# Performance work log

Hardware: AMD Instinct MI355X
Metric: run time of the kernel (lower is better)

## Reference

```python
import jax, jax.numpy as jnp
import numpy as np


def _conv3x3(x, w, b):
    # NCHW conv, stride 1, padding 1 == SAME for 3x3
    y = jax.lax.conv_general_dilated(
        x, w, window_strides=(1, 1), padding='SAME',
        dimension_numbers=('NCHW', 'OIHW', 'NCHW'))
    return y + b[None, :, None, None]


def setup_inputs() -> dict:
    key = jax.random.key(0)
    k_x, k_w1, k_b1, k_w2, k_b2 = jax.random.split(key, 5)
    B, T, C, H, W = 4, 16, 128, 112, 112  # C = 2 * in_channels
    x = jax.random.normal(k_x, (B, T, C, H, W), dtype=jnp.float32)
    # PredictorLG_conv(embed_dim=2*in_channels): Conv2d(128,2,3) -> GELU -> Conv2d(2,2,3) -> GELU -> Softmax(dim=1)
    w1 = jax.random.normal(k_w1, (2, C, 3, 3), dtype=jnp.float32) * 0.05
    b1 = jax.random.normal(k_b1, (2,), dtype=jnp.float32) * 0.05
    w2 = jax.random.normal(k_w2, (2, 2, 3, 3), dtype=jnp.float32) * 0.05
    b2 = jax.random.normal(k_b2, (2,), dtype=jnp.float32) * 0.05
    return {"x": x, "w1": w1, "b1": b1, "w2": w2, "b2": b2}


def reference(x, w1, b1, w2, b2):
    # spatch branch of PatchNet_ms_conv.forward
    B, T, C, H, W = x.shape
    xf = x.reshape(B * T, C, H, W)  # (b t c h w) -> ((b t) c h w)
    s = jax.nn.gelu(_conv3x3(xf, w1, b1), approximate=False)
    s = jax.nn.gelu(_conv3x3(s, w2, b2), approximate=False)
    s = jax.nn.softmax(s, axis=1)  # nn.Softmax() on 4D -> dim=1
    x1, x2 = jnp.split(xf, 2, axis=1)  # chunk(2, dim=-3)
    xa = s[:, 0:1] * x1 + s[:, 1:2] * x2  # ((b t), c//2, h, w)
    # '(b t) c h w -> b c t h w'
    xa = xa.reshape(B, T, C // 2, H, W).transpose(0, 2, 1, 3, 4)
    return xa
```

## Files before the change

### kernel.cpp

```cpp
#include <hip/hip_runtime.h>
#include <math.h>
#include <stdint.h>

#define HW    112
#define HW2   (112 * 112)
#define NIMG  64
#define CIN   128
#define NKG   4
#define ICG   (CIN / NKG)
#define TILEF (18 * HW)
#define TILEP 2032

__device__ __forceinline__ float gelu_exact(float v) {
    return 0.5f * v * (1.0f + erff(v * 0.70710678118654752f));
}

__global__ __launch_bounds__(256) void k1_partial(
    const float* __restrict__ x, const float* __restrict__ w1,
    float* __restrict__ part) {
    __shared__ __align__(16) float tile[2][TILEP];

    const int tid = threadIdx.x;
    const int bx  = blockIdx.x;
    const int n   = blockIdx.y;
    const int kg  = blockIdx.z;
    const int h0  = bx * 16;
    const int icb = kg * ICG;

    const int tx   = tid & 15;
    const int ty   = tid >> 4;
    const int col0 = tx * 7;

    if (bx == 0 && tid < HW) { tile[0][tid] = 0.f; tile[1][tid] = 0.f; }
    if (bx == 6 && tid < HW) { tile[0][17 * HW + tid] = 0.f; tile[1][17 * HW + tid] = 0.f; }

    const int    ldsoff = (bx == 0) ? HW : 0;
    const int    count4 = (bx == 0 || bx == 6) ? 476 : 504;
    const size_t srcoff = (bx == 0) ? 0 : (size_t)(h0 - 1) * HW;
    const float* xn = x + ((size_t)n * CIN + icb) * HW2 + srcoff;

    const float lmask = (col0 > 0) ? 1.f : 0.f;
    const float rmask = (col0 + 7 < HW) ? 1.f : 0.f;
    const int   loff  = (col0 > 0) ? -1 : 0;
    const int   roff  = (col0 + 7 < HW) ? 7 : 0;

    float acc0[7] = {0.f, 0.f, 0.f, 0.f, 0.f, 0.f, 0.f};
    float acc1[7] = {0.f, 0.f, 0.f, 0.f, 0.f, 0.f, 0.f};

    {
        float* dst = &tile[0][ldsoff];
#pragma unroll
        for (int r = 0; r < 2; ++r) {
            const int i = tid + r * 256;
            if (i < count4)
                __builtin_amdgcn_global_load_lds(
                    (const __attribute__((address_space(1))) unsigned int*)(xn + (size_t)i * 4),
                    (__attribute__((address_space(3))) unsigned int*)(dst + i * 4),
                    16, 0, 0);
        }
    }
    __syncthreads();

    int buf = 0;
    for (int ic = 0; ic < ICG; ++ic) {
        if (ic + 1 < ICG) {
            const float* src = xn + (size_t)(ic + 1) * HW2;
            float* dst = &tile[buf ^ 1][ldsoff];
#pragma unroll
            for (int r = 0; r < 2; ++r) {
                const int i = tid + r * 256;
                if (i < count4)
                    __builtin_amdgcn_global_load_lds(
                        (const __attribute__((address_space(1))) unsigned int*)(src + (size_t)i * 4),
                        (__attribute__((address_space(3))) unsigned int*)(dst + i * 4),
                        16, 0, 0);
            }
        }

        const float* wa = w1 + (size_t)(icb + ic) * 9;
        const float* wb = wa + (size_t)CIN * 9;
        const float* tl = tile[buf];
#pragma unroll
        for (int dr = 0; dr < 3; ++dr) {
            const int base = (ty + dr) * HW + col0;
            float v[9];
            v[0] = tl[base + loff] * lmask;
#pragma unroll
            for (int k = 1; k <= 7; ++k) v[k] = tl[base + (k - 1)];
            v[8] = tl[base + roff] * rmask;
            const float a0 = wa[dr * 3 + 0], a1 = wa[dr * 3 + 1], a2 = wa[dr * 3 + 2];
            const float c0 = wb[dr * 3 + 0], c1 = wb[dr * 3 + 1], c2 = wb[dr * 3 + 2];
#pragma unroll
            for (int j = 0; j < 7; ++j) {
                acc0[j] += a0 * v[j] + a1 * v[j + 1] + a2 * v[j + 2];
                acc1[j] += c0 * v[j] + c1 * v[j + 1] + c2 * v[j + 2];
            }
        }

        __syncthreads();
        buf ^= 1;
    }

    const size_t obase = ((size_t)kg * NIMG + n) * 2;
    float* p0 = part + (obase + 0) * HW2 + (size_t)(h0 + ty) * HW + col0;
    float* p1 = part + (obase + 1) * HW2 + (size_t)(h0 + ty) * HW + col0;
#pragma unroll
    for (int j = 0; j < 7; ++j) { p0[j] = acc0[j]; p1[j] = acc1[j]; }
}

__global__ __launch_bounds__(256) void k1b_reduce_gelu(
    const float* __restrict__ part, const float* __restrict__ b1,
    float* __restrict__ g, int total4) {
    int idx = blockIdx.x * blockDim.x + threadIdx.x;
    if (idx >= total4) return;
    const size_t stride = (size_t)NIMG * 2 * HW2;
    const size_t e = (size_t)idx * 4;
    const int oc = (int)((e / HW2) & 1);
    float4 s = *reinterpret_cast<const float4*>(part + e);
#pragma unroll
    for (int kg = 1; kg < NKG; ++kg) {
        const float4 p = *reinterpret_cast<const float4*>(part + kg * stride + e);
        s.x += p.x; s.y += p.y; s.z += p.z; s.w += p.w;
    }
    const float bb = b1[oc];
    float4 o;
    o.x = gelu_exact(s.x + bb);
    o.y = gelu_exact(s.y + bb);
    o.z = gelu_exact(s.z + bb);
    o.w = gelu_exact(s.w + bb);
    *reinterpret_cast<float4*>(g + e) = o;
}

__global__ __launch_bounds__(448) void k1_conv1_gelu(
    const float* __restrict__ x, const float* __restrict__ w1,
    const float* __restrict__ b1, float* __restrict__ g) {
    const int n  = blockIdx.y;
    const int h  = blockIdx.x * 16 + threadIdx.y;
    const int w0 = threadIdx.x * 4;

    float acc0[4], acc1[4];
    const float bb0 = b1[0], bb1 = b1[1];
#pragma unroll
    for (int j = 0; j < 4; ++j) { acc0[j] = bb0; acc1[j] = bb1; }

    const float* xn = x + (size_t)n * CIN * HW2;

#pragma unroll 4
    for (int ic = 0; ic < CIN; ++ic) {
        const float* xc = xn + (size_t)ic * HW2;
        const float* wa = w1 + ic * 9;
        const float* wb = w1 + (CIN + ic) * 9;
#pragma unroll
        for (int dh = -1; dh <= 1; ++dh) {
            const int hh = h + dh;
            if (hh < 0 || hh >= HW) continue;
            const float* xr = xc + hh * HW;
            const float4 c4  = *reinterpret_cast<const float4*>(xr + w0);
            const float left  = (w0 > 0)      ? xr[w0 - 1] : 0.0f;
            const float right = (w0 + 4 < HW) ? xr[w0 + 4] : 0.0f;
            const float v0 = left, v1 = c4.x, v2 = c4.y, v3 = c4.z, v4 = c4.w, v5 = right;
            const int r = (dh + 1) * 3;
            const float a0 = wa[r], a1 = wa[r + 1], a2 = wa[r + 2];
            const float c0 = wb[r], c1 = wb[r + 1], c2 = wb[r + 2];
            acc0[0] += a0 * v0 + a1 * v1 + a2 * v2;
            acc0[1] += a0 * v1 + a1 * v2 + a2 * v3;
            acc0[2] += a0 * v2 + a1 * v3 + a2 * v4;
            acc0[3] += a0 * v3 + a1 * v4 + a2 * v5;
            acc1[0] += c0 * v0 + c1 * v1 + c2 * v2;
            acc1[1] += c0 * v1 + c1 * v2 + c2 * v3;
            acc1[2] += c0 * v2 + c1 * v3 + c2 * v4;
            acc1[3] += c0 * v3 + c1 * v4 + c2 * v5;
        }
    }

    float4 o0, o1;
    o0.x = gelu_exact(acc0[0]); o0.y = gelu_exact(acc0[1]);
    o0.z = gelu_exact(acc0[2]); o0.w = gelu_exact(acc0[3]);
    o1.x = gelu_exact(acc1[0]); o1.y = gelu_exact(acc1[1]);
    o1.z = gelu_exact(acc1[2]); o1.w = gelu_exact(acc1[3]);
    float* g0 = g + (size_t)(n * 2 + 0) * HW2 + h * HW + w0;
    float* g1 = g + (size_t)(n * 2 + 1) * HW2 + h * HW + w0;
    *reinterpret_cast<float4*>(g0) = o0;
    *reinterpret_cast<float4*>(g1) = o1;
}

__global__ __launch_bounds__(448) void k2_conv2_softmax(
    const float* __restrict__ g, const float* __restrict__ w2,
    const float* __restrict__ b2, float* __restrict__ s0) {
    const int n  = blockIdx.y;
    const int h  = blockIdx.x * 16 + threadIdx.y;
    const int w0 = threadIdx.x * 4;

    float accA[4], accB[4];
    const float bb0 = b2[0], bb1 = b2[1];
#pragma unroll
    for (int j = 0; j < 4; ++j) { accA[j] = bb0; accB[j] = bb1; }

#pragma unroll
    for (int c = 0; c < 2; ++c) {
        const float* gc = g + (size_t)(n * 2 + c) * HW2;
        const float* wa = w2 + c * 9;
        const float* wb = w2 + (2 + c) * 9;
#pragma unroll
        for (int dh = -1; dh <= 1; ++dh) {
            const int hh = h + dh;
            if (hh < 0 || hh >= HW) continue;
            const float* gr = gc + hh * HW;
            const float4 c4  = *reinterpret_cast<const float4*>(gr + w0);
            const float left  = (w0 > 0)      ? gr[w0 - 1] : 0.0f;
            const float right = (w0 + 4 < HW) ? gr[w0 + 4] : 0.0f;
            const float v0 = left, v1 = c4.x, v2 = c4.y, v3 = c4.z, v4 = c4.w, v5 = right;
            const int r = (dh + 1) * 3;
            const float a0 = wa[r], a1 = wa[r + 1], a2 = wa[r + 2];
            const float c0 = wb[r], c1 = wb[r + 1], c2 = wb[r + 2];
            accA[0] += a0 * v0 + a1 * v1 + a2 * v2;
            accA[1] += a0 * v1 + a1 * v2 + a2 * v3;
            accA[2] += a0 * v2 + a1 * v3 + a2 * v4;
            accA[3] += a0 * v3 + a1 * v4 + a2 * v5;
            accB[0] += c0 * v0 + c1 * v1 + c2 * v2;
            accB[1] += c0 * v1 + c1 * v2 + c2 * v3;
            accB[2] += c0 * v2 + c1 * v3 + c2 * v4;
            accB[3] += c0 * v3 + c1 * v4 + c2 * v5;
        }
    }

    float4 o;
    o.x = 1.0f / (1.0f + expf(gelu_exact(accB[0]) - gelu_exact(accA[0])));
    o.y = 1.0f / (1.0f + expf(gelu_exact(accB[1]) - gelu_exact(accA[1])));
    o.z = 1.0f / (1.0f + expf(gelu_exact(accB[2]) - gelu_exact(accA[2])));
    o.w = 1.0f / (1.0f + expf(gelu_exact(accB[3]) - gelu_exact(accA[3])));
    *reinterpret_cast<float4*>(s0 + (size_t)n * HW2 + h * HW + w0) = o;
}

__global__ __launch_bounds__(256) void k3_blend(
    const float* __restrict__ x, const float* __restrict__ s0,
    float* __restrict__ out, int total4) {
    int idx = blockIdx.x * blockDim.x + threadIdx.x;
    if (idx >= total4) return;
    const int W4 = HW / 4;
    int w4  = idx % W4;
    int tmp = idx / W4;
    int h   = tmp % HW; tmp /= HW;
    int t   = tmp % 16; tmp /= 16;
    int c   = tmp % 64;
    int b   = tmp / 64;
    const int n = b * 16 + t;

    const size_t px = (size_t)h * HW + w4 * 4;
    const float4 x1 = *reinterpret_cast<const float4*>(x + (size_t)(n * CIN + c)      * HW2 + px);
    const float4 x2 = *reinterpret_cast<const float4*>(x + (size_t)(n * CIN + c + 64) * HW2 + px);
    const float4 s  = *reinterpret_cast<const float4*>(s0 + (size_t)n * HW2 + px);

    float4 o;
    o.x = s.x * x1.x + (1.0f - s.x) * x2.x;
    o.y = s.y * x1.y + (1.0f - s.y) * x2.y;
    o.z = s.z * x1.z + (1.0f - s.z) * x2.z;
    o.w = s.w * x1.w + (1.0f - s.w) * x2.w;
    *reinterpret_cast<float4*>(out + (size_t)idx * 4) = o;
}

extern "C" void kernel_launch(void* const* d_in, const int* in_sizes, int n_in,
                              void* d_out, int out_size, void* d_ws, size_t ws_size,
                              hipStream_t stream) {
    const float* x  = (const float*)d_in[0];
    const float* w1 = (const float*)d_in[1];
    const float* b1 = (const float*)d_in[2];
    const float* w2 = (const float*)d_in[3];
    const float* b2 = (const float*)d_in[4];
    float* out = (float*)d_out;

    const size_t partF = (size_t)NKG * NIMG * 2 * HW2;
    const size_t gF    = (size_t)NIMG * 2 * HW2;
    const size_t s0F   = (size_t)NIMG * HW2;
    const size_t need  = (partF + gF + s0F) * sizeof(float);

    dim3 grd(7, NIMG);

    float *g, *s0;
    if (ws_size >= need) {
        float* part = (float*)d_ws;
        g  = part + partF;
        s0 = g + gF;
        dim3 grdp(7, NIMG, NKG);
        k1_partial<<<grdp, 256, 0, stream>>>(x, w1, part);
        const int total4g = (int)(gF / 4);
        k1b_reduce_gelu<<<(total4g + 255) / 256, 256, 0, stream>>>(part, b1, g, total4g);
    } else {
        g  = (float*)d_ws;
        s0 = g + gF;
        dim3 blk(28, 16);
        k1_conv1_gelu<<<grd, blk, 0, stream>>>(x, w1, b1, g);
    }

    dim3 blk2(28, 16);
    k2_conv2_softmax<<<grd, blk2, 0, stream>>>(g, w2, b2, s0);

    const int total4 = 4 * 64 * 16 * HW * (HW / 4);
    k3_blend<<<(total4 + 255) / 256, 256, 0, stream>>>(x, s0, out, total4);
}
```

Baseline: 209.7 us.

## Fuse conv2/softmax with blend, deepen conv1 LDS pipeline, halve K-split

```diff
diff --git a/kernel.cpp b/kernel.cpp
--- a/kernel.cpp
+++ b/kernel.cpp
@@ -6,10 +6,11 @@
 #define HW2   (112 * 112)
 #define NIMG  64
 #define CIN   128
-#define NKG   4
+#define NKG   2
 #define ICG   (CIN / NKG)
-#define TILEF (18 * HW)
 #define TILEP 2032
+#define NSLOT 4
+#define NWG   (2 * ICG * 9)
 
 __device__ __forceinline__ float gelu_exact(float v) {
     return 0.5f * v * (1.0f + erff(v * 0.70710678118654752f));
@@ -18,7 +19,8 @@
 __global__ __launch_bounds__(256) void k1_partial(
     const float* __restrict__ x, const float* __restrict__ w1,
     float* __restrict__ part) {
-    __shared__ __align__(16) float tile[2][TILEP];
+    __shared__ __align__(16) float tile[NSLOT][TILEP];
+    __shared__ float wlds[NWG];
 
     const int tid = threadIdx.x;
     const int bx  = blockIdx.x;
@@ -31,8 +33,19 @@
     const int ty   = tid >> 4;
     const int col0 = tx * 7;
 
-    if (bx == 0 && tid < HW) { tile[0][tid] = 0.f; tile[1][tid] = 0.f; }
-    if (bx == 6 && tid < HW) { tile[0][17 * HW + tid] = 0.f; tile[1][17 * HW + tid] = 0.f; }
+    for (int j = tid; j < NWG; j += 256) {
+        const int oc   = j / (ICG * 9);
+        const int rest = j - oc * (ICG * 9);
+        wlds[j] = w1[(size_t)oc * CIN * 9 + (size_t)icb * 9 + rest];
+    }
+    if (bx == 0 && tid < HW) {
+#pragma unroll
+        for (int s = 0; s < NSLOT; ++s) tile[s][tid] = 0.f;
+    }
+    if (bx == 6 && tid < HW) {
+#pragma unroll
+        for (int s = 0; s < NSLOT; ++s) tile[s][17 * HW + tid] = 0.f;
+    }
 
     const int    ldsoff = (bx == 0) ? HW : 0;
     const int    count4 = (bx == 0 || bx == 6) ? 476 : 504;
@@ -47,39 +60,40 @@
     float acc0[7] = {0.f, 0.f, 0.f, 0.f, 0.f, 0.f, 0.f};
     float acc1[7] = {0.f, 0.f, 0.f, 0.f, 0.f, 0.f, 0.f};
 
-    {
-        float* dst = &tile[0][ldsoff];
-#pragma unroll
-        for (int r = 0; r < 2; ++r) {
-            const int i = tid + r * 256;
-            if (i < count4)
-                __builtin_amdgcn_global_load_lds(
-                    (const __attribute__((address_space(1))) unsigned int*)(xn + (size_t)i * 4),
-                    (__attribute__((address_space(3))) unsigned int*)(dst + i * 4),
-                    16, 0, 0);
-        }
-    }
-    __syncthreads();
-
-    int buf = 0;
+#define STAGE(CH, SLOT)                                                        \
+    do {                                                                       \
+        const float* _src = xn + (size_t)(CH) * HW2;                           \
+        float* _dst = &tile[(SLOT)][ldsoff];                                   \
+        _Pragma("unroll")                                                      \
+        for (int _r = 0; _r < 2; ++_r) {                                       \
+            const int _i = tid + _r * 256;                                     \
+            if (_i < count4)                                                   \
+                __builtin_amdgcn_global_load_lds(                              \
+                    (const __attribute__((address_space(1))) unsigned int*)(_src + (size_t)_i * 4), \
+                    (__attribute__((address_space(3))) unsigned int*)(_dst + _i * 4), \
+                    16, 0, 0);                                                 \
+        }                                                                      \
+    } while (0)
+
+    STAGE(0, 0);
+    STAGE(1, 1);
+    STAGE(2, 2);
+    STAGE(3, 3);
+    asm volatile("s_waitcnt lgkmcnt(0)" ::: "memory");
+
+    int slot = 0;
+#pragma unroll 1
     for (int ic = 0; ic < ICG; ++ic) {
-        if (ic + 1 < ICG) {
-            const float* src = xn + (size_t)(ic + 1) * HW2;
-            float* dst = &tile[buf ^ 1][ldsoff];
-#pragma unroll
-            for (int r = 0; r < 2; ++r) {
-                const int i = tid + r * 256;
-                if (i < count4)
-                    __builtin_amdgcn_global_load_lds(
-                        (const __attribute__((address_space(1))) unsigned int*)(src + (size_t)i * 4),
-                        (__attribute__((address_space(3))) unsigned int*)(dst + i * 4),
-                        16, 0, 0);
-            }
-        }
-
-        const float* wa = w1 + (size_t)(icb + ic) * 9;
-        const float* wb = wa + (size_t)CIN * 9;
-        const float* tl = tile[buf];
+        if (ic < ICG - 3)       asm volatile("s_waitcnt vmcnt(6)" ::: "memory");
+        else if (ic == ICG - 3) asm volatile("s_waitcnt vmcnt(4)" ::: "memory");
+        else if (ic == ICG - 2) asm volatile("s_waitcnt vmcnt(2)" ::: "memory");
+        else                    asm volatile("s_waitcnt vmcnt(0)" ::: "memory");
+        __builtin_amdgcn_s_barrier();
+        __builtin_amdgcn_sched_barrier(0);
+
+        const float* tl  = tile[slot];
+        const float* wap = wlds + ic * 9;
+        const float* wbp = wlds + ICG * 9 + ic * 9;
 #pragma unroll
         for (int dr = 0; dr < 3; ++dr) {
             const int base = (ty + dr) * HW + col0;
@@ -88,8 +102,8 @@
 #pragma unroll
             for (int k = 1; k <= 7; ++k) v[k] = tl[base + (k - 1)];
             v[8] = tl[base + roff] * rmask;
-            const float a0 = wa[dr * 3 + 0], a1 = wa[dr * 3 + 1], a2 = wa[dr * 3 + 2];
-            const float c0 = wb[dr * 3 + 0], c1 = wb[dr * 3 + 1], c2 = wb[dr * 3 + 2];
+            const float a0 = wap[dr * 3 + 0], a1 = wap[dr * 3 + 1], a2 = wap[dr * 3 + 2];
+            const float c0 = wbp[dr * 3 + 0], c1 = wbp[dr * 3 + 1], c2 = wbp[dr * 3 + 2];
 #pragma unroll
             for (int j = 0; j < 7; ++j) {
                 acc0[j] += a0 * v[j] + a1 * v[j + 1] + a2 * v[j + 2];
@@ -97,9 +111,13 @@
             }
         }
 
-        __syncthreads();
-        buf ^= 1;
-    }
+        asm volatile("s_waitcnt lgkmcnt(0)" ::: "memory");
+        __builtin_amdgcn_sched_barrier(0);
+        __builtin_amdgcn_s_barrier();
+        if (ic + NSLOT < ICG) STAGE(ic + NSLOT, slot);
+        slot = (slot + 1) & (NSLOT - 1);
+    }
+#undef STAGE
 
     const size_t obase = ((size_t)kg * NIMG + n) * 2;
     float* p0 = part + (obase + 0) * HW2 + (size_t)(h0 + ty) * HW + col0;
@@ -137,14 +155,11 @@
     const int n  = blockIdx.y;
     const int h  = blockIdx.x * 16 + threadIdx.y;
     const int w0 = threadIdx.x * 4;
-
     float acc0[4], acc1[4];
     const float bb0 = b1[0], bb1 = b1[1];
 #pragma unroll
     for (int j = 0; j < 4; ++j) { acc0[j] = bb0; acc1[j] = bb1; }
-
     const float* xn = x + (size_t)n * CIN * HW2;
-
 #pragma unroll 4
     for (int ic = 0; ic < CIN; ++ic) {
         const float* xc = xn + (size_t)ic * HW2;
@@ -172,7 +187,6 @@
             acc1[3] += c0 * v3 + c1 * v4 + c2 * v5;
         }
     }
-
     float4 o0, o1;
     o0.x = gelu_exact(acc0[0]); o0.y = gelu_exact(acc0[1]);
     o0.z = gelu_exact(acc0[2]); o0.w = gelu_exact(acc0[3]);
@@ -184,12 +198,37 @@
     *reinterpret_cast<float4*>(g1) = o1;
 }
 
-__global__ __launch_bounds__(448) void k2_conv2_softmax(
+__global__ __launch_bounds__(448) void k23_conv2_blend(
     const float* __restrict__ g, const float* __restrict__ w2,
-    const float* __restrict__ b2, float* __restrict__ s0) {
-    const int n  = blockIdx.y;
-    const int h  = blockIdx.x * 16 + threadIdx.y;
-    const int w0 = threadIdx.x * 4;
+    const float* __restrict__ b2, const float* __restrict__ x,
+    float* __restrict__ out) {
+    __shared__ __align__(16) float gs[2][18 * HW];
+
+    const int tid = threadIdx.x;
+    const int bx  = blockIdx.x;
+    const int n   = blockIdx.y;
+    const int h0  = bx * 16;
+
+    for (int i = tid; i < 1008; i += 448) {
+        const int ch  = i / 504;
+        const int rem = i - ch * 504;
+        const int r   = rem / 28;
+        const int c4  = rem - r * 28;
+        const int hh  = h0 - 1 + r;
+        float4 v = make_float4(0.f, 0.f, 0.f, 0.f);
+        if (hh >= 0 && hh < HW)
+            v = *reinterpret_cast<const float4*>(
+                g + ((size_t)(n * 2 + ch) * HW + hh) * HW + c4 * 4);
+        *reinterpret_cast<float4*>(&gs[ch][r * HW + c4 * 4]) = v;
+    }
+    __syncthreads();
+
+    const int row  = tid / 28;
+    const int col0 = (tid - row * 28) * 4;
+    const float lm = (col0 > 0) ? 1.f : 0.f;
+    const float rm = (col0 + 4 < HW) ? 1.f : 0.f;
+    const int   lo = (col0 > 0) ? -1 : 0;
+    const int   ro = (col0 + 4 < HW) ? 1 : 0;
 
     float accA[4], accB[4];
     const float bb0 = b2[0], bb1 = b2[1];
@@ -197,22 +236,18 @@
     for (int j = 0; j < 4; ++j) { accA[j] = bb0; accB[j] = bb1; }
 
 #pragma unroll
-    for (int c = 0; c < 2; ++c) {
-        const float* gc = g + (size_t)(n * 2 + c) * HW2;
-        const float* wa = w2 + c * 9;
-        const float* wb = w2 + (2 + c) * 9;
-#pragma unroll
-        for (int dh = -1; dh <= 1; ++dh) {
-            const int hh = h + dh;
-            if (hh < 0 || hh >= HW) continue;
-            const float* gr = gc + hh * HW;
-            const float4 c4  = *reinterpret_cast<const float4*>(gr + w0);
-            const float left  = (w0 > 0)      ? gr[w0 - 1] : 0.0f;
-            const float right = (w0 + 4 < HW) ? gr[w0 + 4] : 0.0f;
-            const float v0 = left, v1 = c4.x, v2 = c4.y, v3 = c4.z, v4 = c4.w, v5 = right;
-            const int r = (dh + 1) * 3;
-            const float a0 = wa[r], a1 = wa[r + 1], a2 = wa[r + 2];
-            const float c0 = wb[r], c1 = wb[r + 1], c2 = wb[r + 2];
+    for (int ch = 0; ch < 2; ++ch) {
+        const float* wa = w2 + ch * 9;
+        const float* wb = w2 + (2 + ch) * 9;
+#pragma unroll
+        for (int dr = 0; dr < 3; ++dr) {
+            const int base = (row + dr) * HW + col0;
+            const float4 c4 = *reinterpret_cast<const float4*>(&gs[ch][base]);
+            const float v0 = gs[ch][base + lo] * lm;
+            const float v5 = gs[ch][base + 3 + ro] * rm;
+            const float v1 = c4.x, v2 = c4.y, v3 = c4.z, v4 = c4.w;
+            const float a0 = wa[dr * 3], a1 = wa[dr * 3 + 1], a2 = wa[dr * 3 + 2];
+            const float c0 = wb[dr * 3], c1 = wb[dr * 3 + 1], c2 = wb[dr * 3 + 2];
             accA[0] += a0 * v0 + a1 * v1 + a2 * v2;
             accA[1] += a0 * v1 + a1 * v2 + a2 * v3;
             accA[2] += a0 * v2 + a1 * v3 + a2 * v4;
@@ -224,39 +259,29 @@
         }
     }
 
-    float4 o;
-    o.x = 1.0f / (1.0f + expf(gelu_exact(accB[0]) - gelu_exact(accA[0])));
-    o.y = 1.0f / (1.0f + expf(gelu_exact(accB[1]) - gelu_exact(accA[1])));
-    o.z = 1.0f / (1.0f + expf(gelu_exact(accB[2]) - gelu_exact(accA[2])));
-    o.w = 1.0f / (1.0f + expf(gelu_exact(accB[3]) - gelu_exact(accA[3])));
-    *reinterpret_cast<float4*>(s0 + (size_t)n * HW2 + h * HW + w0) = o;
-}
-
-__global__ __launch_bounds__(256) void k3_blend(
-    const float* __restrict__ x, const float* __restrict__ s0,
-    float* __restrict__ out, int total4) {
-    int idx = blockIdx.x * blockDim.x + threadIdx.x;
-    if (idx >= total4) return;
-    const int W4 = HW / 4;
-    int w4  = idx % W4;
-    int tmp = idx / W4;
-    int h   = tmp % HW; tmp /= HW;
-    int t   = tmp % 16; tmp /= 16;
-    int c   = tmp % 64;
-    int b   = tmp / 64;
-    const int n = b * 16 + t;
-
-    const size_t px = (size_t)h * HW + w4 * 4;
-    const float4 x1 = *reinterpret_cast<const float4*>(x + (size_t)(n * CIN + c)      * HW2 + px);
-    const float4 x2 = *reinterpret_cast<const float4*>(x + (size_t)(n * CIN + c + 64) * HW2 + px);
-    const float4 s  = *reinterpret_cast<const float4*>(s0 + (size_t)n * HW2 + px);
-
-    float4 o;
-    o.x = s.x * x1.x + (1.0f - s.x) * x2.x;
-    o.y = s.y * x1.y + (1.0f - s.y) * x2.y;
-    o.z = s.z * x1.z + (1.0f - s.z) * x2.z;
-    o.w = s.w * x1.w + (1.0f - s.w) * x2.w;
-    *reinterpret_cast<float4*>(out + (size_t)idx * 4) = o;
+    float4 s;
+    s.x = 1.0f / (1.0f + expf(gelu_exact(accB[0]) - gelu_exact(accA[0])));
+    s.y = 1.0f / (1.0f + expf(gelu_exact(accB[1]) - gelu_exact(accA[1])));
+    s.z = 1.0f / (1.0f + expf(gelu_exact(accB[2]) - gelu_exact(accA[2])));
+    s.w = 1.0f / (1.0f + expf(gelu_exact(accB[3]) - gelu_exact(accA[3])));
+
+    const int b = n >> 4, t = n & 15;
+    const size_t px = (size_t)(h0 + row) * HW + col0;
+    const float* x1p = x + ((size_t)n * CIN) * HW2 + px;
+    const float* x2p = x1p + (size_t)64 * HW2;
+    float* op = out + (((size_t)(b * 64) * 16 + t) * HW2) + px;
+#pragma unroll 4
+    for (int c = 0; c < 64; ++c) {
+        const float4 x1 = *reinterpret_cast<const float4*>(x1p);
+        const float4 x2 = *reinterpret_cast<const float4*>(x2p);
+        float4 o;
+        o.x = s.x * x1.x + (1.0f - s.x) * x2.x;
+        o.y = s.y * x1.y + (1.0f - s.y) * x2.y;
+        o.z = s.z * x1.z + (1.0f - s.z) * x2.z;
+        o.w = s.w * x1.w + (1.0f - s.w) * x2.w;
+        *reinterpret_cast<float4*>(op) = o;
+        x1p += HW2; x2p += HW2; op += (size_t)16 * HW2;
+    }
 }
 
 extern "C" void kernel_launch(void* const* d_in, const int* in_sizes, int n_in,
@@ -271,30 +296,23 @@
 
     const size_t partF = (size_t)NKG * NIMG * 2 * HW2;
     const size_t gF    = (size_t)NIMG * 2 * HW2;
-    const size_t s0F   = (size_t)NIMG * HW2;
-    const size_t need  = (partF + gF + s0F) * sizeof(float);
+    const size_t need  = (partF + gF) * sizeof(float);
 
     dim3 grd(7, NIMG);
 
-    float *g, *s0;
+    float* g;
     if (ws_size >= need) {
         float* part = (float*)d_ws;
-        g  = part + partF;
-        s0 = g + gF;
+        g = part + partF;
         dim3 grdp(7, NIMG, NKG);
         k1_partial<<<grdp, 256, 0, stream>>>(x, w1, part);
         const int total4g = (int)(gF / 4);
         k1b_reduce_gelu<<<(total4g + 255) / 256, 256, 0, stream>>>(part, b1, g, total4g);
     } else {
-        g  = (float*)d_ws;
-        s0 = g + gF;
+        g = (float*)d_ws;
         dim3 blk(28, 16);
         k1_conv1_gelu<<<grd, blk, 0, stream>>>(x, w1, b1, g);
     }
 
-    dim3 blk2(28, 16);
-    k2_conv2_softmax<<<grd, blk2, 0, stream>>>(g, w2, b2, s0);
-
-    const int total4 = 4 * 64 * 16 * HW * (HW / 4);
-    k3_blend<<<(total4 + 255) / 256, 256, 0, stream>>>(x, s0, out, total4);
-}
+    k23_conv2_blend<<<grd, 448, 0, stream>>>(g, w2, b2, x, out);
+}
```

Measured after the change: 241.4 us. +15.1%, slower.
